# Optimization experiments

Measured on AMD Instinct MI355X. Metric: run time of the kernel, lower is better.

The kernel has to match this reference:

```python
import jax, jax.numpy as jnp
import numpy as np

B = 4
P0, P1, P2 = 196608, 49152, 12288
DEG = 8
K = 4
EPS = 1e-5


def _cheb_conv(x, cols, vals, W, b):
    """Chebyshev graph conv. x: (B,P,Cin); cols/vals: (P,DEG) fixed-degree sparse L;
    W: (K*Cin, Cout); b: (Cout,). Recursion: T0=x, T1=Lx, Tk=2 L T_{k-1} - T_{k-2}."""
    def lmul(y):  # sparse matvec per batch/channel: (B,P,C) -> (B,P,C)
        return jnp.einsum('pd,bpdc->bpc', vals, y[:, cols, :])
    t0 = x
    t1 = lmul(t0)
    terms = [t0, t1]
    for _ in range(K - 2):
        t2 = 2.0 * lmul(t1) - t0
        terms.append(t2)
        t0, t1 = t1, t2
    xk = jnp.concatenate(terms, axis=-1)  # (B,P,K*Cin)
    return xk @ W + b


def _layernorm(h, g, bt):
    mu = jnp.mean(h, axis=-1, keepdims=True)
    var = jnp.mean(jnp.square(h - mu), axis=-1, keepdims=True)
    return g * (h - mu) / jnp.sqrt(var + EPS) + bt


def _avg_pool4(h):  # HEALPix nested-order average pooling: (B,P,C) -> (B,P//4,C)
    Bh, P, C = h.shape
    return h.reshape(Bh, P // 4, 4, C).mean(axis=2)


def setup_inputs() -> dict:
    key = jax.random.key(0)
    ks = jax.random.split(key, 16)
    cin, c1, c2, c3 = 16, 64, 128, 256
    hid, emb = 512, 256

    def glorot(k, shape):
        fan_in = shape[0]
        return jax.random.normal(k, shape, jnp.float32) / np.sqrt(fan_in)

    inp = {
        'x': jax.random.normal(ks[0], (B, P0, cin), jnp.float32),
        'cols1': jax.random.randint(ks[1], (P0, DEG), 0, P0),
        'vals1': 0.2 * jax.random.normal(ks[2], (P0, DEG), jnp.float32),
        'cols2': jax.random.randint(ks[3], (P1, DEG), 0, P1),
        'vals2': 0.2 * jax.random.normal(ks[4], (P1, DEG), jnp.float32),
        'cols3': jax.random.randint(ks[5], (P2, DEG), 0, P2),
        'vals3': 0.2 * jax.random.normal(ks[6], (P2, DEG), jnp.float32),
        'W1': glorot(ks[7], (K * cin, c1)), 'b1': jnp.zeros((c1,), jnp.float32),
        'g1': jnp.ones((c1,), jnp.float32), 'bt1': jnp.zeros((c1,), jnp.float32),
        'W2': glorot(ks[8], (K * c1, c2)), 'b2': jnp.zeros((c2,), jnp.float32),
        'g2': jnp.ones((c2,), jnp.float32), 'bt2': jnp.zeros((c2,), jnp.float32),
        'W3': glorot(ks[9], (K * c2, c3)), 'b3': jnp.zeros((c3,), jnp.float32),
        'g3': jnp.ones((c3,), jnp.float32), 'bt3': jnp.zeros((c3,), jnp.float32),
        'mW1': glorot(ks[10], (c3, hid)), 'mb1': jnp.zeros((hid,), jnp.float32),
        'mW2': glorot(ks[11], (hid, emb)), 'mb2': jnp.zeros((emb,), jnp.float32),
    }
    return inp


def reference(x, cols1, vals1, cols2, vals2, cols3, vals3,
              W1, b1, g1, bt1, W2, b2, g2, bt2, W3, b3, g3, bt3,
              mW1, mb1, mW2, mb2):
    # Stage 1: ChebConv -> LayerNorm -> ReLU -> avg pool (4:1)
    h = _cheb_conv(x, cols1, vals1, W1, b1)
    h = jax.nn.relu(_layernorm(h, g1, bt1))
    h = _avg_pool4(h)
    # Stage 2
    h = _cheb_conv(h, cols2, vals2, W2, b2)
    h = jax.nn.relu(_layernorm(h, g2, bt2))
    h = _avg_pool4(h)
    # Stage 3 (last stage: no pooling)
    h = _cheb_conv(h, cols3, vals3, W3, b3)
    h = jax.nn.relu(_layernorm(h, g3, bt3))
    # Global mean pool over pixels, then MLP head (Linear-ReLU-Linear)
    z = h.mean(axis=1)                     # (B, 256)
    z = jax.nn.relu(z @ mW1 + mb1)
    z = z @ mW2 + mb2                      # (B, 256)
    return z
```

## Files before the change

kernel.cpp:

```cpp
#include <hip/hip_runtime.h>
#include <hip/hip_bf16.h>

namespace {

constexpr int B  = 4;
constexpr int P0 = 196608, P1 = 49152, P2 = 12288;
constexpr int DEG = 8;
constexpr float EPS = 1e-5f;
constexpr int NCH = 96;
constexpr int CHP = P2 / NCH;

typedef __attribute__((ext_vector_type(4))) float f32x4;
typedef __attribute__((ext_vector_type(8))) short s16x8;

__device__ __forceinline__ float b2f(unsigned short u) {
    union { unsigned int i; float f; } c; c.i = (unsigned int)u << 16; return c.f;
}
__device__ __forceinline__ unsigned short f2b(float f) {
    __hip_bfloat16 h = __float2bfloat16(f);
    return *reinterpret_cast<unsigned short*>(&h);
}

__global__ __launch_bounds__(256)
void x2p_kernel(const float* __restrict__ in, unsigned short* __restrict__ out)
{
    long idx = (long)blockIdx.x * blockDim.x + threadIdx.x;
    if (idx >= (long)P0 * B * 2) return;
    int  h = (int)(idx & 1);
    int  b = (int)((idx >> 1) & 3);
    long p = idx >> 3;
    const float* src = in + ((size_t)b * P0 + p) * 16 + h * 8;
    float4 v0 = *(const float4*)src;
    float4 v1 = *(const float4*)(src + 4);
    union { uint4 u; unsigned short s[8]; } o;
    o.s[0] = f2b(v0.x); o.s[1] = f2b(v0.y); o.s[2] = f2b(v0.z); o.s[3] = f2b(v0.w);
    o.s[4] = f2b(v1.x); o.s[5] = f2b(v1.y); o.s[6] = f2b(v1.z); o.s[7] = f2b(v1.w);
    *(uint4*)&out[((size_t)p * B + b) * 16 + h * 8] = o.u;
}

__global__ __launch_bounds__(256)
void wt_convert_kernel(const float* __restrict__ W, unsigned short* __restrict__ Wt,
                       int K, int N)
{
    int i = blockIdx.x * blockDim.x + threadIdx.x;
    if (i >= K * N) return;
    int n = i % N, k = i / N;
    Wt[(size_t)n * K + k] = f2b(W[i]);
}

__global__ __launch_bounds__(256)
void lmul_bf16_kernel(const unsigned short* __restrict__ in,
                      const unsigned short* __restrict__ prev,
                      const int* __restrict__ cols, const float* __restrict__ vals,
                      unsigned short* __restrict__ out,
                      int P, int Cv8, float alpha, float beta)
{
    long idx = (long)blockIdx.x * blockDim.x + threadIdx.x;
    long total = (long)P * Cv8;
    if (idx >= total) return;
    int v = (int)(idx % Cv8);
    int p = (int)(idx / Cv8);

    const uint4* in16 = (const uint4*)in;
    const int*   cp = cols + p * DEG;
    const float* vp = vals + p * DEG;

    float acc[8] = {0.f,0.f,0.f,0.f,0.f,0.f,0.f,0.f};
#pragma unroll
    for (int d = 0; d < DEG; ++d) {
        int   col = cp[d];
        float w   = vp[d];
        union { uint4 u; unsigned short s[8]; } x;
        x.u = in16[(size_t)col * Cv8 + v];
#pragma unroll
        for (int j = 0; j < 8; ++j) acc[j] = fmaf(w, b2f(x.s[j]), acc[j]);
    }
    size_t o = (size_t)p * Cv8 + v;
    if (beta != 0.f) {
        union { uint4 u; unsigned short s[8]; } pv;
        pv.u = ((const uint4*)prev)[o];
#pragma unroll
        for (int j = 0; j < 8; ++j)
            acc[j] = fmaf(alpha, acc[j], beta * b2f(pv.s[j]));
    } else if (alpha != 1.f) {
#pragma unroll
        for (int j = 0; j < 8; ++j) acc[j] *= alpha;
    }
    union { uint4 u; unsigned short s[8]; } ou;
#pragma unroll
    for (int j = 0; j < 8; ++j) ou.s[j] = f2b(acc[j]);
    ((uint4*)out)[o] = ou.u;
}

template <int CIN, int COUT, int POOL, int LOG2CIN>
__global__ __launch_bounds__(256)
void cheb_mm_mfma_kernel(const unsigned short* __restrict__ t0,
                         const unsigned short* __restrict__ t1,
                         const unsigned short* __restrict__ t2,
                         const unsigned short* __restrict__ t3,
                         const unsigned short* __restrict__ Wt,
                         const float* __restrict__ bias,
                         const float* __restrict__ gam,
                         const float* __restrict__ bet,
                         void* __restrict__ outv)
{
    constexpr int KC   = 4 * CIN;
    constexpr int NF   = COUT / 16;
    constexpr int NKCH = KC / 64;
    constexpr int LDA  = 72;

    __shared__ unsigned short As[64 * LDA];
    __shared__ unsigned short Ws[COUT * LDA];

    const int tid  = threadIdx.x;
    const int pblk = blockIdx.x * 16;
    const int wave = tid >> 6;
    const int lane = tid & 63;
    const int g    = lane >> 4;
    const int c16  = lane & 15;

    f32x4 acc[NF];
#pragma unroll
    for (int n = 0; n < NF; ++n) {
        float bz = bias[n * 16 + c16];
        acc[n] = (f32x4){bz, bz, bz, bz};
    }

    for (int kc = 0; kc < NKCH; ++kc) {
        if (kc) __syncthreads();
#pragma unroll
        for (int i = tid; i < 64 * 8; i += 256) {
            int row = i >> 3, v = i & 7;
            int k = kc * 64 + v * 8;
            int t = k >> LOG2CIN;
            int c = k & (CIN - 1);
            int pix = pblk + ((row >> 4) << 2) + (row & 3);
            int bb  = (row >> 2) & 3;
            const unsigned short* src =
                (t == 0) ? t0 : (t == 1) ? t1 : (t == 2) ? t2 : t3;
            *(uint4*)&As[row * LDA + v * 8] =
                *(const uint4*)&src[((size_t)pix * B + bb) * CIN + c];
        }
#pragma unroll
        for (int i = tid; i < COUT * 8; i += 256) {
            int co = i >> 3, v = i & 7;
            *(uint4*)&Ws[co * LDA + v * 8] =
                *(const uint4*)&Wt[(size_t)co * KC + kc * 64 + v * 8];
        }
        __syncthreads();
#pragma unroll
        for (int ks = 0; ks < 2; ++ks) {
            s16x8 a = *(const s16x8*)&As[(wave * 16 + c16) * LDA + ks * 32 + g * 8];
#pragma unroll
            for (int n = 0; n < NF; ++n) {
                s16x8 bf = *(const s16x8*)&Ws[(n * 16 + c16) * LDA + ks * 32 + g * 8];
                acc[n] = __builtin_amdgcn_mfma_f32_16x16x32_bf16(a, bf, acc[n], 0, 0, 0);
            }
        }
    }

    float s[4] = {0,0,0,0}, q[4] = {0,0,0,0};
#pragma unroll
    for (int n = 0; n < NF; ++n)
#pragma unroll
        for (int r = 0; r < 4; ++r) {
            float v = acc[n][r];
            s[r] += v; q[r] += v * v;
        }
#pragma unroll
    for (int msk = 1; msk < 16; msk <<= 1)
#pragma unroll
        for (int r = 0; r < 4; ++r) {
            s[r] += __shfl_xor(s[r], msk, 64);
            q[r] += __shfl_xor(q[r], msk, 64);
        }
    float mu[4], rs[4];
#pragma unroll
    for (int r = 0; r < 4; ++r) {
        mu[r] = s[r] * (1.f / COUT);
        float var = q[r] * (1.f / COUT) - mu[r] * mu[r];
        rs[r] = rsqrtf(var + EPS);
    }

    if constexpr (POOL == 4) {
        unsigned short* out = (unsigned short*)outv;
        size_t rowo = ((size_t)(blockIdx.x * 4 + wave) * B + g) * COUT;
#pragma unroll
        for (int n = 0; n < NF; ++n) {
            float gv = gam[n * 16 + c16], bv = bet[n * 16 + c16];
            float pv = 0.f;
#pragma unroll
            for (int r = 0; r < 4; ++r) {
                float h = fmaf(gv * rs[r], acc[n][r] - mu[r], bv);
                pv += fmaxf(h, 0.f);
            }
            out[rowo + n * 16 + c16] = f2b(pv * 0.25f);
        }
    } else {
        float* out = (float*)outv;
#pragma unroll
        for (int n = 0; n < NF; ++n) {
            float gv = gam[n * 16 + c16], bv = bet[n * 16 + c16];
#pragma unroll
            for (int r = 0; r < 4; ++r) {
                float h = fmaf(gv * rs[r], acc[n][r] - mu[r], bv);
                out[((size_t)(pblk + wave * 4 + r) * B + g) * COUT + n * 16 + c16] =
                    fmaxf(h, 0.f);
            }
        }
    }
}

__global__ __launch_bounds__(256)
void colsum_kernel(const float* __restrict__ h, float* __restrict__ zpart)
{
    int blk = blockIdx.x;
    int b   = blk / NCH, ch = blk % NCH;
    int c   = threadIdx.x;
    const float* __restrict__ base =
        h + ((size_t)(ch * CHP) * B + b) * 256 + c;
    float s = 0.f;
#pragma unroll 4
    for (int p = 0; p < CHP; ++p) s += base[(size_t)p * B * 256];
    zpart[((size_t)(b * NCH + ch)) * 256 + c] = s;
}

__global__ __launch_bounds__(512)
void head_kernel(const float* __restrict__ zpart,
                 const float* __restrict__ mW1, const float* __restrict__ mb1,
                 const float* __restrict__ mW2, const float* __restrict__ mb2,
                 float* __restrict__ out)
{
    __shared__ float zs[256];
    __shared__ float hsh[512];
    int b = blockIdx.x, tid = threadIdx.x;
    if (tid < 256) {
        float s = 0.f;
        for (int ch = 0; ch < NCH; ++ch)
            s += zpart[((size_t)(b * NCH + ch)) * 256 + tid];
        zs[tid] = s * (1.0f / P2);
    }
    __syncthreads();
    {
        float a = mb1[tid];
#pragma unroll 8
        for (int i = 0; i < 256; ++i) a = fmaf(zs[i], mW1[i * 512 + tid], a);
        hsh[tid] = fmaxf(a, 0.f);
    }
    __syncthreads();
    if (tid < 256) {
        float a = mb2[tid];
#pragma unroll 8
        for (int i = 0; i < 512; ++i) a = fmaf(hsh[i], mW2[i * 256 + tid], a);
        out[(size_t)b * 256 + tid] = a;
    }
}

}

extern "C" void kernel_launch(void* const* d_in, const int* in_sizes, int n_in,
                              void* d_out, int out_size, void* d_ws, size_t ws_size,
                              hipStream_t stream)
{
    const float* x     = (const float*)d_in[0];
    const int*   cols1 = (const int*)  d_in[1];
    const float* vals1 = (const float*)d_in[2];
    const int*   cols2 = (const int*)  d_in[3];
    const float* vals2 = (const float*)d_in[4];
    const int*   cols3 = (const int*)  d_in[5];
    const float* vals3 = (const float*)d_in[6];
    const float* W1  = (const float*)d_in[7];
    const float* b1  = (const float*)d_in[8];
    const float* g1  = (const float*)d_in[9];
    const float* bt1 = (const float*)d_in[10];
    const float* W2  = (const float*)d_in[11];
    const float* b2  = (const float*)d_in[12];
    const float* g2  = (const float*)d_in[13];
    const float* bt2 = (const float*)d_in[14];
    const float* W3  = (const float*)d_in[15];
    const float* b3  = (const float*)d_in[16];
    const float* g3  = (const float*)d_in[17];
    const float* bt3 = (const float*)d_in[18];
    const float* mW1 = (const float*)d_in[19];
    const float* mb1 = (const float*)d_in[20];
    const float* mW2 = (const float*)d_in[21];
    const float* mb2 = (const float*)d_in[22];
    float* out = (float*)d_out;

    char* w = (char*)d_ws;
    size_t off = 0;
    auto alloc = [&](size_t bytes) -> void* {
        void* p = w + off;
        off += (bytes + 255) & ~(size_t)255;
        return p;
    };
    const size_t E1 = (size_t)B * P0 * 16;
    unsigned short* xb  = (unsigned short*)alloc(E1 * 2);
    unsigned short* t_a = (unsigned short*)alloc(E1 * 2);
    unsigned short* t_b = (unsigned short*)alloc(E1 * 2);
    unsigned short* t_c = (unsigned short*)alloc(E1 * 2);
    unsigned short* h1  = (unsigned short*)alloc((size_t)P1 * B * 64 * 2);
    unsigned short* h2  = (unsigned short*)alloc((size_t)P2 * B * 128 * 2);
    float*          h3  = (float*)alloc((size_t)P2 * B * 256 * 4);
    unsigned short* Wt1 = (unsigned short*)alloc(64 * 64 * 2);
    unsigned short* Wt2 = (unsigned short*)alloc(256 * 128 * 2);
    unsigned short* Wt3 = (unsigned short*)alloc(512 * 256 * 2);
    float*        zpart = (float*)alloc((size_t)B * NCH * 256 * 4);

    x2p_kernel<<<(int)(((long)P0 * B * 2 + 255) / 256), 256, 0, stream>>>(x, xb);
    wt_convert_kernel<<<(64 * 64 + 255) / 256, 256, 0, stream>>>(W1, Wt1, 64, 64);
    wt_convert_kernel<<<(256 * 128 + 255) / 256, 256, 0, stream>>>(W2, Wt2, 256, 128);
    wt_convert_kernel<<<(512 * 256 + 255) / 256, 256, 0, stream>>>(W3, Wt3, 512, 256);

    {
        int Cv8 = B * 16 / 8;
        long tot = (long)P0 * Cv8;
        int nb = (int)((tot + 255) / 256);
        lmul_bf16_kernel<<<nb, 256, 0, stream>>>(xb,  nullptr, cols1, vals1, t_a, P0, Cv8, 1.f,  0.f);
        lmul_bf16_kernel<<<nb, 256, 0, stream>>>(t_a, xb,      cols1, vals1, t_b, P0, Cv8, 2.f, -1.f);
        lmul_bf16_kernel<<<nb, 256, 0, stream>>>(t_b, t_a,     cols1, vals1, t_c, P0, Cv8, 2.f, -1.f);
        cheb_mm_mfma_kernel<16, 64, 4, 4><<<P0 / 16, 256, 0, stream>>>(
            xb, t_a, t_b, t_c, Wt1, b1, g1, bt1, h1);
    }
    {
        int Cv8 = B * 64 / 8;
        long tot = (long)P1 * Cv8;
        int nb = (int)((tot + 255) / 256);
        lmul_bf16_kernel<<<nb, 256, 0, stream>>>(h1,  nullptr, cols2, vals2, t_a, P1, Cv8, 1.f,  0.f);
        lmul_bf16_kernel<<<nb, 256, 0, stream>>>(t_a, h1,      cols2, vals2, t_b, P1, Cv8, 2.f, -1.f);
        lmul_bf16_kernel<<<nb, 256, 0, stream>>>(t_b, t_a,     cols2, vals2, t_c, P1, Cv8, 2.f, -1.f);
        cheb_mm_mfma_kernel<64, 128, 4, 6><<<P1 / 16, 256, 0, stream>>>(
            h1, t_a, t_b, t_c, Wt2, b2, g2, bt2, h2);
    }
    {
        int Cv8 = B * 128 / 8;
        long tot = (long)P2 * Cv8;
        int nb = (int)((tot + 255) / 256);
        lmul_bf16_kernel<<<nb, 256, 0, stream>>>(h2,  nullptr, cols3, vals3, t_a, P2, Cv8, 1.f,  0.f);
        lmul_bf16_kernel<<<nb, 256, 0, stream>>>(t_a, h2,      cols3, vals3, t_b, P2, Cv8, 2.f, -1.f);
        lmul_bf16_kernel<<<nb, 256, 0, stream>>>(t_b, t_a,     cols3, vals3, t_c, P2, Cv8, 2.f, -1.f);
        cheb_mm_mfma_kernel<128, 256, 1, 7><<<P2 / 16, 256, 0, stream>>>(
            h2, t_a, t_b, t_c, Wt3, b3, g3, bt3, h3);
    }
    colsum_kernel<<<B * NCH, 256, 0, stream>>>(h3, zpart);
    head_kernel<<<B, 512, 0, stream>>>(zpart, mW1, mb1, mW2, mb2, out);

    (void)in_sizes; (void)n_in; (void)out_size; (void)ws_size;
}
```

Baseline: 464.6 us.

## Specialize stage-1 matmul, retile stage-2/3 matmuls, fuse global pooling into stage 3

Adds a stage-1 matmul kernel that keeps the 64x64 weight fragments in registers and loops over pixel tiles grid-stride, with no LDS staging. Stages 2 and 3 are retiled so each block computes 64 rows and each wave owns a quarter of the output columns. The layernorm statistics are then reduced across waves through shared memory. Stage 3 no longer writes the full fp32 activation tensor; it writes per-block column partial sums that the head kernel reduces, which removes the colsum kernel. The three weight-conversion launches are merged into one. The cost is more partial sums for the head to read serially, plus an extra block-level sync for the row statistics.

Measured after the change: 459.8 us. No clear change (-1.0%).

```diff
diff --git a/kernel.cpp b/kernel.cpp
--- a/kernel.cpp
+++ b/kernel.cpp
@@ -7,8 +7,7 @@
 constexpr int P0 = 196608, P1 = 49152, P2 = 12288;
 constexpr int DEG = 8;
 constexpr float EPS = 1e-5f;
-constexpr int NCH = 96;
-constexpr int CHP = P2 / NCH;
+constexpr int NBLK3 = (P2 * B) / 64;
 
 typedef __attribute__((ext_vector_type(4))) float f32x4;
 typedef __attribute__((ext_vector_type(8))) short s16x8;
@@ -39,13 +38,24 @@
 }
 
 __global__ __launch_bounds__(256)
-void wt_convert_kernel(const float* __restrict__ W, unsigned short* __restrict__ Wt,
-                       int K, int N)
-{
-    int i = blockIdx.x * blockDim.x + threadIdx.x;
-    if (i >= K * N) return;
-    int n = i % N, k = i / N;
-    Wt[(size_t)n * K + k] = f2b(W[i]);
+void wt_all_kernel(const float* __restrict__ W1, const float* __restrict__ W2,
+                   const float* __restrict__ W3,
+                   unsigned short* __restrict__ Wt1, unsigned short* __restrict__ Wt2,
+                   unsigned short* __restrict__ Wt3)
+{
+    int i = blockIdx.x * 256 + threadIdx.x;
+    if (i < 4096) {
+        int n = i % 64, k = i / 64;
+        Wt1[n * 64 + k] = f2b(W1[i]);
+    } else if (i < 4096 + 32768) {
+        int j = i - 4096;
+        int n = j % 128, k = j / 128;
+        Wt2[n * 256 + k] = f2b(W2[j]);
+    } else if (i < 4096 + 32768 + 131072) {
+        int j = i - 36864;
+        int n = j % 256, k = j / 256;
+        Wt3[n * 512 + k] = f2b(W3[j]);
+    }
 }
 
 __global__ __launch_bounds__(256)
@@ -92,39 +102,142 @@
     ((uint4*)out)[o] = ou.u;
 }
 
+__global__ __launch_bounds__(256)
+void s1_mm_kernel(const unsigned short* __restrict__ t0,
+                  const unsigned short* __restrict__ t1,
+                  const unsigned short* __restrict__ t2,
+                  const unsigned short* __restrict__ t3,
+                  const unsigned short* __restrict__ Wt,
+                  const float* __restrict__ bias,
+                  const float* __restrict__ gam,
+                  const float* __restrict__ bet,
+                  unsigned short* __restrict__ out)
+{
+    const int wave = threadIdx.x >> 6;
+    const int lane = threadIdx.x & 63;
+    const int g    = lane >> 4;
+    const int c16  = lane & 15;
+
+    s16x8 wf[2][4];
+#pragma unroll
+    for (int ks = 0; ks < 2; ++ks)
+#pragma unroll
+        for (int n = 0; n < 4; ++n)
+            wf[ks][n] = *(const s16x8*)&Wt[(size_t)(n * 16 + c16) * 64 + ks * 32 + g * 8];
+
+    float bz[4], gz[4], tz[4];
+#pragma unroll
+    for (int n = 0; n < 4; ++n) {
+        bz[n] = bias[n * 16 + c16];
+        gz[n] = gam [n * 16 + c16];
+        tz[n] = bet [n * 16 + c16];
+    }
+
+    const unsigned short* tb[4] = { t0, t1, t2, t3 };
+    const int term0  = g >> 1;
+    const int coloff = (g & 1) * 8;
+    const int bb     = c16 >> 2;
+    const int px     = c16 & 3;
+
+    constexpr int NT = P0 / 4;
+    const int wg     = blockIdx.x * 4 + wave;
+    const int wstep  = gridDim.x * 4;
+
+    for (int t = wg; t < NT; t += wstep) {
+        size_t rowbase = ((size_t)(t * 4 + px) * 4 + bb) * 16 + coloff;
+        s16x8 a0 = *(const s16x8*)&tb[term0    ][rowbase];
+        s16x8 a1 = *(const s16x8*)&tb[term0 + 2][rowbase];
+
+        f32x4 acc[4];
+#pragma unroll
+        for (int n = 0; n < 4; ++n) acc[n] = (f32x4){bz[n], bz[n], bz[n], bz[n]};
+#pragma unroll
+        for (int n = 0; n < 4; ++n)
+            acc[n] = __builtin_amdgcn_mfma_f32_16x16x32_bf16(a0, wf[0][n], acc[n], 0, 0, 0);
+#pragma unroll
+        for (int n = 0; n < 4; ++n)
+            acc[n] = __builtin_amdgcn_mfma_f32_16x16x32_bf16(a1, wf[1][n], acc[n], 0, 0, 0);
+
+        float s[4] = {0,0,0,0}, q[4] = {0,0,0,0};
+#pragma unroll
+        for (int n = 0; n < 4; ++n)
+#pragma unroll
+            for (int r = 0; r < 4; ++r) {
+                float v = acc[n][r];
+                s[r] += v; q[r] += v * v;
+            }
+#pragma unroll
+        for (int msk = 1; msk < 16; msk <<= 1)
+#pragma unroll
+            for (int r = 0; r < 4; ++r) {
+                s[r] += __shfl_xor(s[r], msk, 64);
+                q[r] += __shfl_xor(q[r], msk, 64);
+            }
+        float mu[4], rs[4];
+#pragma unroll
+        for (int r = 0; r < 4; ++r) {
+            mu[r] = s[r] * (1.f / 64.f);
+            float var = q[r] * (1.f / 64.f) - mu[r] * mu[r];
+            rs[r] = rsqrtf(var + EPS);
+        }
+        size_t ro = ((size_t)t * 4 + g) * 64;
+#pragma unroll
+        for (int n = 0; n < 4; ++n) {
+            float pv = 0.f;
+#pragma unroll
+            for (int r = 0; r < 4; ++r) {
+                float h = fmaf(gz[n] * rs[r], acc[n][r] - mu[r], tz[n]);
+                pv += fmaxf(h, 0.f);
+            }
+            out[ro + n * 16 + c16] = f2b(pv * 0.25f);
+        }
+    }
+}
+
 template <int CIN, int COUT, int POOL, int LOG2CIN>
 __global__ __launch_bounds__(256)
-void cheb_mm_mfma_kernel(const unsigned short* __restrict__ t0,
-                         const unsigned short* __restrict__ t1,
-                         const unsigned short* __restrict__ t2,
-                         const unsigned short* __restrict__ t3,
-                         const unsigned short* __restrict__ Wt,
-                         const float* __restrict__ bias,
-                         const float* __restrict__ gam,
-                         const float* __restrict__ bet,
-                         void* __restrict__ outv)
+void cheb_mm_v2_kernel(const unsigned short* __restrict__ t0,
+                       const unsigned short* __restrict__ t1,
+                       const unsigned short* __restrict__ t2,
+                       const unsigned short* __restrict__ t3,
+                       const unsigned short* __restrict__ Wt,
+                       const float* __restrict__ bias,
+                       const float* __restrict__ gam,
+                       const float* __restrict__ bet,
+                       void* __restrict__ outv)
 {
     constexpr int KC   = 4 * CIN;
-    constexpr int NF   = COUT / 16;
+    constexpr int WNF  = COUT / 64;
     constexpr int NKCH = KC / 64;
     constexpr int LDA  = 72;
 
     __shared__ unsigned short As[64 * LDA];
     __shared__ unsigned short Ws[COUT * LDA];
+    __shared__ float sq[64][4][2];
 
     const int tid  = threadIdx.x;
-    const int pblk = blockIdx.x * 16;
     const int wave = tid >> 6;
     const int lane = tid & 63;
     const int g    = lane >> 4;
     const int c16  = lane & 15;
-
-    f32x4 acc[NF];
-#pragma unroll
-    for (int n = 0; n < NF; ++n) {
-        float bz = bias[n * 16 + c16];
-        acc[n] = (f32x4){bz, bz, bz, bz};
-    }
+    const int wcol = wave * (COUT / 4);
+
+    const unsigned short* tb[4] = { t0, t1, t2, t3 };
+
+    float bz[WNF], gz[WNF], tz[WNF];
+#pragma unroll
+    for (int n = 0; n < WNF; ++n) {
+        bz[n] = bias[wcol + n * 16 + c16];
+        gz[n] = gam [wcol + n * 16 + c16];
+        tz[n] = bet [wcol + n * 16 + c16];
+    }
+
+    f32x4 acc[4][WNF];
+#pragma unroll
+    for (int m = 0; m < 4; ++m)
+#pragma unroll
+        for (int n = 0; n < WNF; ++n)
+            acc[m][n] = (f32x4){bz[n], bz[n], bz[n], bz[n]};
 
     for (int kc = 0; kc < NKCH; ++kc) {
         if (kc) __syncthreads();
@@ -132,14 +245,17 @@
         for (int i = tid; i < 64 * 8; i += 256) {
             int row = i >> 3, v = i & 7;
             int k = kc * 64 + v * 8;
-            int t = k >> LOG2CIN;
+            int term = k >> LOG2CIN;
             int c = k & (CIN - 1);
-            int pix = pblk + ((row >> 4) << 2) + (row & 3);
-            int bb  = (row >> 2) & 3;
-            const unsigned short* src =
-                (t == 0) ? t0 : (t == 1) ? t1 : (t == 2) ? t2 : t3;
-            *(uint4*)&As[row * LDA + v * 8] =
-                *(const uint4*)&src[((size_t)pix * B + bb) * CIN + c];
+            size_t srow;
+            if constexpr (POOL == 4) {
+                int pix = blockIdx.x * 16 + ((row >> 4) << 2) + (row & 3);
+                int rb  = (row >> 2) & 3;
+                srow = ((size_t)pix * B + rb) * CIN + c;
+            } else {
+                srow = ((size_t)(blockIdx.x * 64 + row)) * CIN + c;
+            }
+            *(uint4*)&As[row * LDA + v * 8] = *(const uint4*)&tb[term][srow];
         }
 #pragma unroll
         for (int i = tid; i < COUT * 8; i += 256) {
@@ -150,83 +266,118 @@
         __syncthreads();
 #pragma unroll
         for (int ks = 0; ks < 2; ++ks) {
-            s16x8 a = *(const s16x8*)&As[(wave * 16 + c16) * LDA + ks * 32 + g * 8];
-#pragma unroll
-            for (int n = 0; n < NF; ++n) {
-                s16x8 bf = *(const s16x8*)&Ws[(n * 16 + c16) * LDA + ks * 32 + g * 8];
-                acc[n] = __builtin_amdgcn_mfma_f32_16x16x32_bf16(a, bf, acc[n], 0, 0, 0);
-            }
-        }
-    }
-
-    float s[4] = {0,0,0,0}, q[4] = {0,0,0,0};
-#pragma unroll
-    for (int n = 0; n < NF; ++n)
+            s16x8 a[4];
+#pragma unroll
+            for (int m = 0; m < 4; ++m)
+                a[m] = *(const s16x8*)&As[(m * 16 + c16) * LDA + ks * 32 + g * 8];
+#pragma unroll
+            for (int n = 0; n < WNF; ++n) {
+                s16x8 bf = *(const s16x8*)&Ws[(wcol + n * 16 + c16) * LDA + ks * 32 + g * 8];
+#pragma unroll
+                for (int m = 0; m < 4; ++m)
+                    acc[m][n] = __builtin_amdgcn_mfma_f32_16x16x32_bf16(a[m], bf, acc[m][n], 0, 0, 0);
+            }
+        }
+    }
+
+    float sm[4][4], qm[4][4];
+#pragma unroll
+    for (int m = 0; m < 4; ++m)
+#pragma unroll
+        for (int r = 0; r < 4; ++r) { sm[m][r] = 0.f; qm[m][r] = 0.f; }
+#pragma unroll
+    for (int m = 0; m < 4; ++m)
+#pragma unroll
+        for (int n = 0; n < WNF; ++n)
+#pragma unroll
+            for (int r = 0; r < 4; ++r) {
+                float v = acc[m][n][r];
+                sm[m][r] += v; qm[m][r] += v * v;
+            }
+#pragma unroll
+    for (int msk = 1; msk < 16; msk <<= 1)
+#pragma unroll
+        for (int m = 0; m < 4; ++m)
+#pragma unroll
+            for (int r = 0; r < 4; ++r) {
+                sm[m][r] += __shfl_xor(sm[m][r], msk, 64);
+                qm[m][r] += __shfl_xor(qm[m][r], msk, 64);
+            }
+    __syncthreads();
+    if (c16 == 0) {
+#pragma unroll
+        for (int m = 0; m < 4; ++m)
+#pragma unroll
+            for (int r = 0; r < 4; ++r) {
+                sq[m * 16 + g * 4 + r][wave][0] = sm[m][r];
+                sq[m * 16 + g * 4 + r][wave][1] = qm[m][r];
+            }
+    }
+    __syncthreads();
+    float mu[4][4], rs[4][4];
+#pragma unroll
+    for (int m = 0; m < 4; ++m)
 #pragma unroll
         for (int r = 0; r < 4; ++r) {
-            float v = acc[n][r];
-            s[r] += v; q[r] += v * v;
-        }
-#pragma unroll
-    for (int msk = 1; msk < 16; msk <<= 1)
-#pragma unroll
-        for (int r = 0; r < 4; ++r) {
-            s[r] += __shfl_xor(s[r], msk, 64);
-            q[r] += __shfl_xor(q[r], msk, 64);
-        }
-    float mu[4], rs[4];
-#pragma unroll
-    for (int r = 0; r < 4; ++r) {
-        mu[r] = s[r] * (1.f / COUT);
-        float var = q[r] * (1.f / COUT) - mu[r] * mu[r];
-        rs[r] = rsqrtf(var + EPS);
-    }
+            int row = m * 16 + g * 4 + r;
+            float ss = sq[row][0][0] + sq[row][1][0] + sq[row][2][0] + sq[row][3][0];
+            float qq = sq[row][0][1] + sq[row][1][1] + sq[row][2][1] + sq[row][3][1];
+            mu[m][r] = ss * (1.f / COUT);
+            float var = qq * (1.f / COUT) - mu[m][r] * mu[m][r];
+            rs[m][r] = rsqrtf(var + EPS);
+        }
 
     if constexpr (POOL == 4) {
         unsigned short* out = (unsigned short*)outv;
-        size_t rowo = ((size_t)(blockIdx.x * 4 + wave) * B + g) * COUT;
-#pragma unroll
-        for (int n = 0; n < NF; ++n) {
-            float gv = gam[n * 16 + c16], bv = bet[n * 16 + c16];
-            float pv = 0.f;
-#pragma unroll
-            for (int r = 0; r < 4; ++r) {
-                float h = fmaf(gv * rs[r], acc[n][r] - mu[r], bv);
-                pv += fmaxf(h, 0.f);
-            }
-            out[rowo + n * 16 + c16] = f2b(pv * 0.25f);
+#pragma unroll
+        for (int m = 0; m < 4; ++m) {
+            size_t ro = ((size_t)(blockIdx.x * 4 + m) * B + g) * COUT + wcol;
+#pragma unroll
+            for (int n = 0; n < WNF; ++n) {
+                float pv = 0.f;
+#pragma unroll
+                for (int r = 0; r < 4; ++r) {
+                    float h = fmaf(gz[n] * rs[m][r], acc[m][n][r] - mu[m][r], tz[n]);
+                    pv += fmaxf(h, 0.f);
+                }
+                out[ro + n * 16 + c16] = f2b(pv * 0.25f);
+            }
         }
     } else {
-        float* out = (float*)outv;
-#pragma unroll
-        for (int n = 0; n < NF; ++n) {
-            float gv = gam[n * 16 + c16], bv = bet[n * 16 + c16];
-#pragma unroll
-            for (int r = 0; r < 4; ++r) {
-                float h = fmaf(gv * rs[r], acc[n][r] - mu[r], bv);
-                out[((size_t)(pblk + wave * 4 + r) * B + g) * COUT + n * 16 + c16] =
-                    fmaxf(h, 0.f);
-            }
-        }
-    }
-}
-
-__global__ __launch_bounds__(256)
-void colsum_kernel(const float* __restrict__ h, float* __restrict__ zpart)
-{
-    int blk = blockIdx.x;
-    int b   = blk / NCH, ch = blk % NCH;
-    int c   = threadIdx.x;
-    const float* __restrict__ base =
-        h + ((size_t)(ch * CHP) * B + b) * 256 + c;
-    float s = 0.f;
-#pragma unroll 4
-    for (int p = 0; p < CHP; ++p) s += base[(size_t)p * B * 256];
-    zpart[((size_t)(b * NCH + ch)) * 256 + c] = s;
+        float part[WNF][4];
+#pragma unroll
+        for (int n = 0; n < WNF; ++n)
+#pragma unroll
+            for (int r = 0; r < 4; ++r) part[n][r] = 0.f;
+#pragma unroll
+        for (int m = 0; m < 4; ++m)
+#pragma unroll
+            for (int n = 0; n < WNF; ++n)
+#pragma unroll
+                for (int r = 0; r < 4; ++r) {
+                    float h = fmaf(gz[n] * rs[m][r], acc[m][n][r] - mu[m][r], tz[n]);
+                    part[n][r] += fmaxf(h, 0.f);
+                }
+#pragma unroll
+        for (int n = 0; n < WNF; ++n)
+#pragma unroll
+            for (int r = 0; r < 4; ++r) {
+                part[n][r] += __shfl_xor(part[n][r], 16, 64);
+                part[n][r] += __shfl_xor(part[n][r], 32, 64);
+            }
+        if (g == 0) {
+            float* zb = (float*)outv + (size_t)blockIdx.x * B * COUT;
+#pragma unroll
+            for (int n = 0; n < WNF; ++n)
+#pragma unroll
+                for (int r = 0; r < 4; ++r)
+                    zb[(size_t)r * COUT + wcol + n * 16 + c16] = part[n][r];
+        }
+    }
 }
 
 __global__ __launch_bounds__(512)
-void head_kernel(const float* __restrict__ zpart,
+void head_kernel(const float* __restrict__ zblk,
                  const float* __restrict__ mW1, const float* __restrict__ mb1,
                  const float* __restrict__ mW2, const float* __restrict__ mb2,
                  float* __restrict__ out)
@@ -236,8 +387,8 @@
     int b = blockIdx.x, tid = threadIdx.x;
     if (tid < 256) {
         float s = 0.f;
-        for (int ch = 0; ch < NCH; ++ch)
-            s += zpart[((size_t)(b * NCH + ch)) * 256 + tid];
+        for (int blk = 0; blk < NBLK3; ++blk)
+            s += zblk[(size_t)blk * B * 256 + (size_t)b * 256 + tid];
         zs[tid] = s * (1.0f / P2);
     }
     __syncthreads();
@@ -301,16 +452,14 @@
     unsigned short* t_c = (unsigned short*)alloc(E1 * 2);
     unsigned short* h1  = (unsigned short*)alloc((size_t)P1 * B * 64 * 2);
     unsigned short* h2  = (unsigned short*)alloc((size_t)P2 * B * 128 * 2);
-    float*          h3  = (float*)alloc((size_t)P2 * B * 256 * 4);
     unsigned short* Wt1 = (unsigned short*)alloc(64 * 64 * 2);
     unsigned short* Wt2 = (unsigned short*)alloc(256 * 128 * 2);
     unsigned short* Wt3 = (unsigned short*)alloc(512 * 256 * 2);
-    float*        zpart = (float*)alloc((size_t)B * NCH * 256 * 4);
+    float*          zblk = (float*)alloc((size_t)NBLK3 * B * 256 * 4);
 
     x2p_kernel<<<(int)(((long)P0 * B * 2 + 255) / 256), 256, 0, stream>>>(x, xb);
-    wt_convert_kernel<<<(64 * 64 + 255) / 256, 256, 0, stream>>>(W1, Wt1, 64, 64);
-    wt_convert_kernel<<<(256 * 128 + 255) / 256, 256, 0, stream>>>(W2, Wt2, 256, 128);
-    wt_convert_kernel<<<(512 * 256 + 255) / 256, 256, 0, stream>>>(W3, Wt3, 512, 256);
+    wt_all_kernel<<<(4096 + 32768 + 131072 + 255) / 256, 256, 0, stream>>>(
+        W1, W2, W3, Wt1, Wt2, Wt3);
 
     {
         int Cv8 = B * 16 / 8;
@@ -319,8 +468,7 @@
         lmul_bf16_kernel<<<nb, 256, 0, stream>>>(xb,  nullptr, cols1, vals1, t_a, P0, Cv8, 1.f,  0.f);
         lmul_bf16_kernel<<<nb, 256, 0, stream>>>(t_a, xb,      cols1, vals1, t_b, P0, Cv8, 2.f, -1.f);
         lmul_bf16_kernel<<<nb, 256, 0, stream>>>(t_b, t_a,     cols1, vals1, t_c, P0, Cv8, 2.f, -1.f);
-        cheb_mm_mfma_kernel<16, 64, 4, 4><<<P0 / 16, 256, 0, stream>>>(
-            xb, t_a, t_b, t_c, Wt1, b1, g1, bt1, h1);
+        s1_mm_kernel<<<2048, 256, 0, stream>>>(xb, t_a, t_b, t_c, Wt1, b1, g1, bt1, h1);
     }
     {
         int Cv8 = B * 64 / 8;
@@ -329,7 +477,7 @@
         lmul_bf16_kernel<<<nb, 256, 0, stream>>>(h1,  nullptr, cols2, vals2, t_a, P1, Cv8, 1.f,  0.f);
         lmul_bf16_kernel<<<nb, 256, 0, stream>>>(t_a, h1,      cols2, vals2, t_b, P1, Cv8, 2.f, -1.f);
         lmul_bf16_kernel<<<nb, 256, 0, stream>>>(t_b, t_a,     cols2, vals2, t_c, P1, Cv8, 2.f, -1.f);
-        cheb_mm_mfma_kernel<64, 128, 4, 6><<<P1 / 16, 256, 0, stream>>>(
+        cheb_mm_v2_kernel<64, 128, 4, 6><<<(P1 * B) / 64, 256, 0, stream>>>(
             h1, t_a, t_b, t_c, Wt2, b2, g2, bt2, h2);
     }
     {
@@ -339,11 +487,10 @@
         lmul_bf16_kernel<<<nb, 256, 0, stream>>>(h2,  nullptr, cols3, vals3, t_a, P2, Cv8, 1.f,  0.f);
         lmul_bf16_kernel<<<nb, 256, 0, stream>>>(t_a, h2,      cols3, vals3, t_b, P2, Cv8, 2.f, -1.f);
         lmul_bf16_kernel<<<nb, 256, 0, stream>>>(t_b, t_a,     cols3, vals3, t_c, P2, Cv8, 2.f, -1.f);
-        cheb_mm_mfma_kernel<128, 256, 1, 7><<<P2 / 16, 256, 0, stream>>>(
-            h2, t_a, t_b, t_c, Wt3, b3, g3, bt3, h3);
-    }
-    colsum_kernel<<<B * NCH, 256, 0, stream>>>(h3, zpart);
-    head_kernel<<<B, 512, 0, stream>>>(zpart, mW1, mb1, mW2, mb2, out);
+        cheb_mm_v2_kernel<128, 256, 1, 7><<<NBLK3, 256, 0, stream>>>(
+            h2, t_a, t_b, t_c, Wt3, b3, g3, bt3, zblk);
+    }
+    head_kernel<<<B, 512, 0, stream>>>(zblk, mW1, mb1, mW2, mb2, out);
 
     (void)in_sizes; (void)n_in; (void)out_size; (void)ws_size;
 }
```
